# Optimization experiments

Measured on AMD Instinct MI355X. Metric: run time of the kernel, lower is better.

## Reference

```python
import jax, jax.numpy as jnp
import numpy as np

N = 50000          # nodes
E = 800000         # directed edges
C = 64             # hidden width = n_clusters
K = 20             # SSGConv propagation hops
RATIO = 30         # TopKPooling ratio (int -> keep 30 nodes)
ALPHAS = (0.7, 0.7, 0.35, 0.7 / 3.0, 0.175)  # 0.7 then 0.7/(i+1)


def setup_inputs() -> dict:
    key = jax.random.key(0)
    ks = jax.random.split(key, 20)
    inp = {
        'x': jax.random.normal(ks[0], (N, 8), dtype=jnp.float32),
        'edge_index': jax.random.randint(ks[1], (2, E), 0, N, dtype=jnp.int32),
        'W0': 0.1 * jax.random.normal(ks[2], (C, 4), dtype=jnp.float32),
        'b0': 0.1 * jax.random.normal(ks[3], (C,), dtype=jnp.float32),
        'W1': 0.1 * jax.random.normal(ks[4], (C, C), dtype=jnp.float32),
        'b1': 0.1 * jax.random.normal(ks[5], (C,), dtype=jnp.float32),
        'W2': 0.1 * jax.random.normal(ks[6], (C, C), dtype=jnp.float32),
        'b2': 0.1 * jax.random.normal(ks[7], (C,), dtype=jnp.float32),
        'W3': 0.1 * jax.random.normal(ks[8], (C, C), dtype=jnp.float32),
        'b3': 0.1 * jax.random.normal(ks[9], (C,), dtype=jnp.float32),
        'W4': 0.1 * jax.random.normal(ks[10], (C, C), dtype=jnp.float32),
        'b4': 0.1 * jax.random.normal(ks[11], (C,), dtype=jnp.float32),
        'Wm': 0.1 * jax.random.normal(ks[12], (C, C), dtype=jnp.float32),
        'bm': 0.1 * jax.random.normal(ks[13], (C,), dtype=jnp.float32),
        'wp': 0.1 * jax.random.normal(ks[14], (C,), dtype=jnp.float32),
    }
    return inp


def _gcn_norm(edge_index, n):
    # add self loops (fill value 1), symmetric normalization D^-1/2 A D^-1/2
    loops = jnp.arange(n, dtype=edge_index.dtype)
    row = jnp.concatenate([edge_index[0], loops])  # source j
    col = jnp.concatenate([edge_index[1], loops])  # target i
    w = jnp.ones(row.shape[0], dtype=jnp.float32)
    deg = jax.ops.segment_sum(w, col, num_segments=n)
    dinv = jnp.where(deg > 0, jax.lax.rsqrt(deg), 0.0)
    return row, col, dinv[row] * dinv[col]


def _ssg(x, row, col, norm, n, alpha, W, b):
    # SSGConv: h = alpha*x + (1-alpha)/K * sum_k A_norm^k x; then Linear
    coef = (1.0 - alpha) / K

    def body(carry, _):
        xk, h = carry
        xk = jax.ops.segment_sum(xk[row] * norm[:, None], col, num_segments=n)
        return (xk, h + coef * xk), None

    (_, h), _ = jax.lax.scan(body, (x, alpha * x), None, length=K)
    return h @ W.T + b


def reference(x, edge_index, W0, b0, W1, b1, W2, b2, W3, b3, W4, b4, Wm, bm, wp):
    x = x[:, :4]
    row, col, norm = _gcn_norm(edge_index, N)
    relu = jax.nn.relu
    x = relu(_ssg(x, row, col, norm, N, ALPHAS[0], W0, b0))
    x = relu(_ssg(x, row, col, norm, N, ALPHAS[1], W1, b1))
    x = relu(_ssg(x, row, col, norm, N, ALPHAS[2], W2, b2)) + x
    x = relu(_ssg(x, row, col, norm, N, ALPHAS[3], W3, b3)) + x
    x = relu(_ssg(x, row, col, norm, N, ALPHAS[4], W4, b4)) + x
    # MLP (mlp_units=[], mlp_act=Identity): single Linear to n_clusters==C
    x = x @ Wm.T + bm
    # TopKPooling: tanh-normalized projection score, keep top RATIO nodes
    score = jnp.tanh((x @ wp) / jnp.linalg.norm(wp))
    top_score, perm = jax.lax.top_k(score, RATIO)
    xp = x[perm] * top_score[:, None]  # [RATIO, C]
    # global_max_pool over the single graph
    return jnp.max(xp, axis=0, keepdims=True)  # [1, C]
```

## Files before the change

### kernel.cpp

```cpp
#include <hip/hip_runtime.h>
#include <hip/hip_fp16.h>
#include <cstdint>
#include <cstddef>

#define NN 50000
#define EE 800000
#define NNZ (NN + EE)
#define KK 20
#define TPK 30
#define P1B 64
#define P1CH ((NN + P1B - 1) / P1B)
#define SCB 256
#define SCNB ((NN + SCB - 1) / SCB)


__device__ __forceinline__ float2 h2f(unsigned int u) {
  __half2 h = *reinterpret_cast<__half2*>(&u);
  return __half22float2(h);
}
__device__ __forceinline__ unsigned int f2h(float a, float b) {
  __half2 h = __floats2half2_rn(a, b);
  return *reinterpret_cast<unsigned int*>(&h);
}


__global__ __launch_bounds__(256) void init_deg(int* deg) {
  int t = blockIdx.x * 256 + threadIdx.x;
  if (t < NN) deg[t] = 1;
}

__global__ __launch_bounds__(256) void count_deg(const int* __restrict__ ecol, int* deg) {
  int t = blockIdx.x * 256 + threadIdx.x;
  if (t < EE) atomicAdd(&deg[ecol[t]], 1);
}

__global__ __launch_bounds__(256) void scan_bsum(const int* __restrict__ deg, int* __restrict__ bsum) {
  __shared__ int red[256];
  int tid = threadIdx.x;
  int t = blockIdx.x * 256 + tid;
  red[tid] = (t < NN) ? deg[t] : 0;
  __syncthreads();
  for (int o = 128; o > 0; o >>= 1) {
    if (tid < o) red[tid] += red[tid + o];
    __syncthreads();
  }
  if (tid == 0) bsum[blockIdx.x] = red[0];
}

__global__ __launch_bounds__(256) void scan_boff(const int* __restrict__ bsum, int* __restrict__ boff) {
  __shared__ int s[256];
  int tid = threadIdx.x;
  int own = (tid < SCNB) ? bsum[tid] : 0;
  s[tid] = own;
  __syncthreads();
  for (int o = 1; o < 256; o <<= 1) {
    int v = s[tid];
    int u = (tid >= o) ? s[tid - o] : 0;
    __syncthreads();
    s[tid] = v + u;
    __syncthreads();
  }
  if (tid < SCNB) boff[tid] = s[tid] - own;
}

__global__ __launch_bounds__(256) void scan_write(const int* __restrict__ deg,
                                                  const int* __restrict__ boff,
                                                  int* __restrict__ rowptr, int* __restrict__ cursor,
                                                  float* __restrict__ dinv) {
  __shared__ int s[256];
  int tid = threadIdx.x;
  int t = blockIdx.x * 256 + tid;
  int d = (t < NN) ? deg[t] : 0;
  s[tid] = d;
  __syncthreads();
  for (int o = 1; o < 256; o <<= 1) {
    int v = s[tid];
    int u = (tid >= o) ? s[tid - o] : 0;
    __syncthreads();
    s[tid] = v + u;
    __syncthreads();
  }
  if (t < NN) {
    int excl = boff[blockIdx.x] + s[tid] - d;
    rowptr[t] = excl;
    cursor[t] = excl;
    dinv[t] = 1.0f / sqrtf((float)d);
    if (t == NN - 1) rowptr[NN] = excl + d;
  }
}

__global__ __launch_bounds__(256) void scatter_csr(const int* __restrict__ erow,
                                                   const int* __restrict__ ecol,
                                                   const float* __restrict__ dinv, int* cursor,
                                                   int2* __restrict__ meta) {
  int t = blockIdx.x * 256 + threadIdx.x;
  if (t < EE) {
    int r = erow[t], c = ecol[t];
    int p = atomicAdd(&cursor[c], 1);
    meta[p] = make_int2(r, __float_as_int(dinv[r] * dinv[c]));
  } else if (t < NNZ) {
    int i = t - EE;
    int p = atomicAdd(&cursor[i], 1);
    meta[p] = make_int2(i, __float_as_int(dinv[i] * dinv[i]));
  }
}

__global__ __launch_bounds__(256) void extract_x0(const float* __restrict__ x, float4* __restrict__ x0) {
  int t = blockIdx.x * 256 + threadIdx.x;
  if (t < NN) x0[t] = *(const float4*)&x[(size_t)t * 8];
}


__global__ __launch_bounds__(256) void sweep64h(const uint4* __restrict__ tinq,
                                                const uint4* __restrict__ xinq,
                                                const float4* __restrict__ xinf,
                                                uint4* __restrict__ touth,
                                                float4* __restrict__ toutf,
                                                const int* __restrict__ rowptr,
                                                const int2* __restrict__ meta,
                                                float aacc, float axc, int isFinal) {
  int lane = threadIdx.x & 63;
  int w = threadIdx.x >> 6;
  int v = blockIdx.x * 4 + w;
  if (v >= NN) return;
  int c8 = lane & 7;
  int e8 = lane >> 3;
  int s = rowptr[v], e = rowptr[v + 1];
  float a0 = 0.f, a1 = 0.f, a2 = 0.f, a3 = 0.f;
  float a4 = 0.f, a5 = 0.f, a6 = 0.f, a7 = 0.f;
  for (int base = s; base < e; base += 64) {
    int nj = e - base;
    if (nj > 64) nj = 64;
    int2 mL = (lane < nj) ? meta[base + lane] : make_int2(0, 0);
    int T = (nj + 7) >> 3;
    int t = 0;
    for (; t + 1 < T; t += 2) {
      int j0 = e8 + 8 * t;
      int j1 = j0 + 8;
      int s0 = __shfl(mL.x, j0);
      int s1 = __shfl(mL.x, j1);
      float w0 = __int_as_float(__shfl(mL.y, j0));
      float w1 = __int_as_float(__shfl(mL.y, j1));
      uint4 q0 = tinq[(size_t)s0 * 8 + c8];
      uint4 q1 = tinq[(size_t)s1 * 8 + c8];
      float2 f;
      f = h2f(q0.x); a0 = fmaf(w0, f.x, a0); a1 = fmaf(w0, f.y, a1);
      f = h2f(q0.y); a2 = fmaf(w0, f.x, a2); a3 = fmaf(w0, f.y, a3);
      f = h2f(q0.z); a4 = fmaf(w0, f.x, a4); a5 = fmaf(w0, f.y, a5);
      f = h2f(q0.w); a6 = fmaf(w0, f.x, a6); a7 = fmaf(w0, f.y, a7);
      f = h2f(q1.x); a0 = fmaf(w1, f.x, a0); a1 = fmaf(w1, f.y, a1);
      f = h2f(q1.y); a2 = fmaf(w1, f.x, a2); a3 = fmaf(w1, f.y, a3);
      f = h2f(q1.z); a4 = fmaf(w1, f.x, a4); a5 = fmaf(w1, f.y, a5);
      f = h2f(q1.w); a6 = fmaf(w1, f.x, a6); a7 = fmaf(w1, f.y, a7);
    }
    if (t < T) {
      int j0 = e8 + 8 * t;
      int s0 = __shfl(mL.x, j0);
      float w0 = __int_as_float(__shfl(mL.y, j0));
      uint4 q0 = tinq[(size_t)s0 * 8 + c8];
      float2 f;
      f = h2f(q0.x); a0 = fmaf(w0, f.x, a0); a1 = fmaf(w0, f.y, a1);
      f = h2f(q0.y); a2 = fmaf(w0, f.x, a2); a3 = fmaf(w0, f.y, a3);
      f = h2f(q0.z); a4 = fmaf(w0, f.x, a4); a5 = fmaf(w0, f.y, a5);
      f = h2f(q0.w); a6 = fmaf(w0, f.x, a6); a7 = fmaf(w0, f.y, a7);
    }
  }
#pragma unroll
  for (int o = 8; o <= 32; o <<= 1) {
    a0 += __shfl_xor(a0, o); a1 += __shfl_xor(a1, o);
    a2 += __shfl_xor(a2, o); a3 += __shfl_xor(a3, o);
    a4 += __shfl_xor(a4, o); a5 += __shfl_xor(a5, o);
    a6 += __shfl_xor(a6, o); a7 += __shfl_xor(a7, o);
  }
  if (e8 == 0) {
    if (isFinal) {
      float4 x0v = xinf[(size_t)v * 16 + c8 * 2];
      float4 x1v = xinf[(size_t)v * 16 + c8 * 2 + 1];
      float4 r0, r1;
      r0.x = aacc * a0 + axc * x0v.x; r0.y = aacc * a1 + axc * x0v.y;
      r0.z = aacc * a2 + axc * x0v.z; r0.w = aacc * a3 + axc * x0v.w;
      r1.x = aacc * a4 + axc * x1v.x; r1.y = aacc * a5 + axc * x1v.y;
      r1.z = aacc * a6 + axc * x1v.z; r1.w = aacc * a7 + axc * x1v.w;
      toutf[(size_t)v * 16 + c8 * 2] = r0;
      toutf[(size_t)v * 16 + c8 * 2 + 1] = r1;
    } else {
      uint4 xq = xinq[(size_t)v * 8 + c8];
      float2 f;
      f = h2f(xq.x); float o0 = a0 + f.x, o1 = a1 + f.y;
      f = h2f(xq.y); float o2 = a2 + f.x, o3 = a3 + f.y;
      f = h2f(xq.z); float o4 = a4 + f.x, o5 = a5 + f.y;
      f = h2f(xq.w); float o6 = a6 + f.x, o7 = a7 + f.y;
      uint4 r;
      r.x = f2h(o0, o1); r.y = f2h(o2, o3);
      r.z = f2h(o4, o5); r.w = f2h(o6, o7);
      touth[(size_t)v * 8 + c8] = r;
    }
  }
}

__global__ __launch_bounds__(256) void sweep4(const float4* __restrict__ tin,
                                              const float4* __restrict__ xin,
                                              float4* __restrict__ tout,
                                              const int* __restrict__ rowptr,
                                              const int2* __restrict__ meta,
                                              float aacc, float axc) {
  int lane = threadIdx.x & 63;
  int w = threadIdx.x >> 6;
  int n16 = lane & 15;
  int e4 = lane >> 4;
  int v = (blockIdx.x * 4 + w) * 16 + n16;
  int vv = (v < NN) ? v : (NN - 1);
  int s = rowptr[vv], e = rowptr[vv + 1];
  float a0 = 0.f, a1 = 0.f, a2 = 0.f, a3 = 0.f;
  float b0 = 0.f, b1 = 0.f, b2 = 0.f, b3 = 0.f;
  int i = s + e4;
  for (; i + 12 < e; i += 16) {
    int2 m0 = meta[i];
    int2 m1 = meta[i + 4];
    int2 m2 = meta[i + 8];
    int2 m3 = meta[i + 12];
    float w0 = __int_as_float(m0.y);
    float w1 = __int_as_float(m1.y);
    float w2 = __int_as_float(m2.y);
    float w3 = __int_as_float(m3.y);
    float4 t0 = tin[m0.x];
    float4 t1 = tin[m1.x];
    float4 t2 = tin[m2.x];
    float4 t3 = tin[m3.x];
    a0 = fmaf(w0, t0.x, a0); a1 = fmaf(w0, t0.y, a1);
    a2 = fmaf(w0, t0.z, a2); a3 = fmaf(w0, t0.w, a3);
    b0 = fmaf(w1, t1.x, b0); b1 = fmaf(w1, t1.y, b1);
    b2 = fmaf(w1, t1.z, b2); b3 = fmaf(w1, t1.w, b3);
    a0 = fmaf(w2, t2.x, a0); a1 = fmaf(w2, t2.y, a1);
    a2 = fmaf(w2, t2.z, a2); a3 = fmaf(w2, t2.w, a3);
    b0 = fmaf(w3, t3.x, b0); b1 = fmaf(w3, t3.y, b1);
    b2 = fmaf(w3, t3.z, b2); b3 = fmaf(w3, t3.w, b3);
  }
  for (; i < e; i += 4) {
    int2 m0 = meta[i];
    float w0 = __int_as_float(m0.y);
    float4 t0 = tin[m0.x];
    a0 = fmaf(w0, t0.x, a0); a1 = fmaf(w0, t0.y, a1);
    a2 = fmaf(w0, t0.z, a2); a3 = fmaf(w0, t0.w, a3);
  }
  a0 += b0; a1 += b1; a2 += b2; a3 += b3;
  a0 += __shfl_xor(a0, 16); a1 += __shfl_xor(a1, 16);
  a2 += __shfl_xor(a2, 16); a3 += __shfl_xor(a3, 16);
  a0 += __shfl_xor(a0, 32); a1 += __shfl_xor(a1, 32);
  a2 += __shfl_xor(a2, 32); a3 += __shfl_xor(a3, 32);
  if (e4 == 0 && v < NN) {
    float4 xv = xin[v];
    float4 o;
    o.x = aacc * a0 + axc * xv.x;
    o.y = aacc * a1 + axc * xv.y;
    o.z = aacc * a2 + axc * xv.z;
    o.w = aacc * a3 + axc * xv.w;
    tout[v] = o;
  }
}


__global__ __launch_bounds__(256) void dense4(const float* __restrict__ h4,
                                              const float* __restrict__ W,
                                              const float* __restrict__ b,
                                              float* __restrict__ out,
                                              unsigned int* __restrict__ outh) {
  __shared__ float sWt[4 * 64];
  int tid = threadIdx.x;
  {
    int j = tid >> 2, c = tid & 3;
    sWt[c * 64 + j] = W[tid];
  }
  __syncthreads();
  int lane = tid & 63, w = tid >> 6;
  int n = blockIdx.x * 4 + w;
  if (n >= NN) return;
  float acc = b[lane];
#pragma unroll
  for (int c = 0; c < 4; ++c)
    acc = fmaf(h4[(size_t)n * 4 + c], sWt[c * 64 + lane], acc);
  acc = fmaxf(acc, 0.f);
  out[(size_t)n * 64 + lane] = acc;
  int p = lane & 31;
  float va = __shfl(acc, 2 * p);
  float vb = __shfl(acc, 2 * p + 1);
  if (lane < 32) outh[(size_t)n * 32 + lane] = f2h(va, vb);
}

#define DN 128
__global__ __launch_bounds__(256) void dense64(const float* __restrict__ h,
                                               const float* __restrict__ W,
                                               const float* __restrict__ b,
                                               const float* __restrict__ resid,
                                               float* __restrict__ out,
                                               uint4* __restrict__ outh,
                                               int doRelu, int doResid) {
  __shared__ float sX[64 * 130];
  __shared__ float sWt[64 * 68];
  int tid = threadIdx.x;
  int base = blockIdx.x * DN;
  for (int i = tid; i < 64 * 64; i += 256) {
    int o = i >> 6, c = i & 63;
    sWt[c * 68 + o] = W[i];
  }
  for (int i = tid; i < DN * 64; i += 256) {
    int node = i >> 6, c = i & 63;
    int n = base + node;
    sX[c * 130 + node] = (n < NN) ? h[(size_t)n * 64 + c] : 0.f;
  }
  __syncthreads();
  int j = tid & 63;
  int q = tid >> 6;
  float acc0[16], acc1[16];
#pragma unroll
  for (int o = 0; o < 16; ++o) { acc0[o] = b[q * 16 + o]; acc1[o] = acc0[o]; }
  for (int c = 0; c < 64; ++c) {
    float x0 = sX[c * 130 + j];
    float x1 = sX[c * 130 + 64 + j];
#pragma unroll
    for (int o4 = 0; o4 < 4; ++o4) {
      float4 wv = *(const float4*)&sWt[c * 68 + q * 16 + o4 * 4];
      acc0[o4 * 4 + 0] = fmaf(x0, wv.x, acc0[o4 * 4 + 0]);
      acc0[o4 * 4 + 1] = fmaf(x0, wv.y, acc0[o4 * 4 + 1]);
      acc0[o4 * 4 + 2] = fmaf(x0, wv.z, acc0[o4 * 4 + 2]);
      acc0[o4 * 4 + 3] = fmaf(x0, wv.w, acc0[o4 * 4 + 3]);
      acc1[o4 * 4 + 0] = fmaf(x1, wv.x, acc1[o4 * 4 + 0]);
      acc1[o4 * 4 + 1] = fmaf(x1, wv.y, acc1[o4 * 4 + 1]);
      acc1[o4 * 4 + 2] = fmaf(x1, wv.z, acc1[o4 * 4 + 2]);
      acc1[o4 * 4 + 3] = fmaf(x1, wv.w, acc1[o4 * 4 + 3]);
    }
  }
  int n0 = base + j, n1 = base + 64 + j;
#pragma unroll
  for (int half = 0; half < 2; ++half) {
    int n = half ? n1 : n0;
    float* acc = half ? acc1 : acc0;
    if (n < NN) {
      if (doRelu) {
#pragma unroll
        for (int o = 0; o < 16; ++o) acc[o] = fmaxf(acc[o], 0.f);
      }
      if (doResid) {
#pragma unroll
        for (int o4 = 0; o4 < 4; ++o4) {
          float4 rv = *(const float4*)&resid[(size_t)n * 64 + q * 16 + o4 * 4];
          acc[o4 * 4 + 0] += rv.x; acc[o4 * 4 + 1] += rv.y;
          acc[o4 * 4 + 2] += rv.z; acc[o4 * 4 + 3] += rv.w;
        }
      }
#pragma unroll
      for (int o4 = 0; o4 < 4; ++o4) {
        float4 r;
        r.x = acc[o4 * 4 + 0]; r.y = acc[o4 * 4 + 1];
        r.z = acc[o4 * 4 + 2]; r.w = acc[o4 * 4 + 3];
        *(float4*)&out[(size_t)n * 64 + q * 16 + o4 * 4] = r;
      }
      if (outh) {
        uint4 u;
        u.x = f2h(acc[0], acc[1]);  u.y = f2h(acc[2], acc[3]);
        u.z = f2h(acc[4], acc[5]);  u.w = f2h(acc[6], acc[7]);
        outh[(size_t)n * 8 + q * 2] = u;
        u.x = f2h(acc[8], acc[9]);  u.y = f2h(acc[10], acc[11]);
        u.z = f2h(acc[12], acc[13]); u.w = f2h(acc[14], acc[15]);
        outh[(size_t)n * 8 + q * 2 + 1] = u;
      }
    }
  }
}


__global__ __launch_bounds__(256) void score_k(const float* __restrict__ y,
                                               const float* __restrict__ wp,
                                               float* __restrict__ scores) {
  int tid = threadIdx.x;
  int lane = tid & 63, w = tid >> 6;
  int n = blockIdx.x * 4 + w;
  if (n >= NN) return;
  float wv = wp[lane];
  float s = wv * wv;
#pragma unroll
  for (int o = 32; o > 0; o >>= 1) s += __shfl_xor(s, o);
  float invn = 1.0f / sqrtf(s);
  float p = y[(size_t)n * 64 + lane] * wv;
#pragma unroll
  for (int o = 32; o > 0; o >>= 1) p += __shfl_xor(p, o);
  if (lane == 0) scores[n] = tanhf(p * invn);
}

__device__ __forceinline__ bool lexgt(float v1, int i1, float v2, int i2) {
  return (v1 > v2) || (v1 == v2 && i1 < i2);
}

__global__ __launch_bounds__(64, 1) void topk_p1(const float* __restrict__ score,
                                                 float* __restrict__ candv,
                                                 int* __restrict__ candi) {
  int lane = threadIdx.x;
  int base = blockIdx.x * P1CH;
  float lv[TPK]; int li[TPK];
#pragma unroll
  for (int k = 0; k < TPK; ++k) { lv[k] = -3.4e38f; li[k] = 0x7FFFFFFF; }
  for (int k = lane; k < P1CH; k += 64) {
    int idx = base + k;
    if (idx >= NN) break;
    float v = score[idx];
    if (lexgt(v, idx, lv[TPK - 1], li[TPK - 1])) {
      float cv = v; int ci = idx;
#pragma unroll
      for (int m = 0; m < TPK; ++m) {
        bool sw = lexgt(cv, ci, lv[m], li[m]);
        float tv = sw ? lv[m] : cv; int ti = sw ? li[m] : ci;
        lv[m] = sw ? cv : lv[m]; li[m] = sw ? ci : li[m];
        cv = tv; ci = ti;
      }
    }
  }
  for (int r = 0; r < TPK; ++r) {
    float bv = lv[0]; int bi = li[0];
#pragma unroll
    for (int o = 32; o > 0; o >>= 1) {
      float ov = __shfl_xor(bv, o); int oi = __shfl_xor(bi, o);
      if (lexgt(ov, oi, bv, bi)) { bv = ov; bi = oi; }
    }
    if (lane == 0) { candv[blockIdx.x * TPK + r] = bv; candi[blockIdx.x * TPK + r] = bi; }
    bool mine = (li[0] == bi);
#pragma unroll
    for (int m = 0; m < TPK - 1; ++m) {
      lv[m] = mine ? lv[m + 1] : lv[m];
      li[m] = mine ? li[m + 1] : li[m];
    }
    if (mine) { lv[TPK - 1] = -3.4e38f; li[TPK - 1] = 0x7FFFFFFF; }
  }
}

__global__ __launch_bounds__(64, 1) void topk_p2_final(const float* __restrict__ candv,
                                                       const int* __restrict__ candi,
                                                       const float* __restrict__ y,
                                                       float* __restrict__ out) {
  __shared__ float sV[TPK];
  __shared__ int sI[TPK];
  int lane = threadIdx.x;
  float lv[TPK]; int li[TPK];
#pragma unroll
  for (int k = 0; k < TPK; ++k) { lv[k] = -3.4e38f; li[k] = 0x7FFFFFFF; }
  for (int k = lane; k < P1B * TPK; k += 64) {
    float v = candv[k]; int id = candi[k];
    if (lexgt(v, id, lv[TPK - 1], li[TPK - 1])) {
      float cv = v; int ci = id;
#pragma unroll
      for (int m = 0; m < TPK; ++m) {
        bool sw = lexgt(cv, ci, lv[m], li[m]);
        float tv = sw ? lv[m] : cv; int ti = sw ? li[m] : ci;
        lv[m] = sw ? cv : lv[m]; li[m] = sw ? ci : li[m];
        cv = tv; ci = ti;
      }
    }
  }
  for (int r = 0; r < TPK; ++r) {
    float bv = lv[0]; int bi = li[0];
#pragma unroll
    for (int o = 32; o > 0; o >>= 1) {
      float ov = __shfl_xor(bv, o); int oi = __shfl_xor(bi, o);
      if (lexgt(ov, oi, bv, bi)) { bv = ov; bi = oi; }
    }
    if (lane == 0) { sV[r] = bv; sI[r] = bi; }
    bool mine = (li[0] == bi);
#pragma unroll
    for (int m = 0; m < TPK - 1; ++m) {
      lv[m] = mine ? lv[m + 1] : lv[m];
      li[m] = mine ? li[m + 1] : li[m];
    }
    if (mine) { lv[TPK - 1] = -3.4e38f; li[TPK - 1] = 0x7FFFFFFF; }
  }
  __syncthreads();
  float m = -3.4e38f;
  for (int r = 0; r < TPK; ++r)
    m = fmaxf(m, y[(size_t)sI[r] * 64 + lane] * sV[r]);
  out[lane] = m;
}


extern "C" void kernel_launch(void* const* d_in, const int* in_sizes, int n_in,
                              void* d_out, int out_size, void* d_ws, size_t ws_size,
                              hipStream_t stream) {
  const float* x = (const float*)d_in[0];
  const int* ei = (const int*)d_in[1];
  const float* Wl[5] = {(const float*)d_in[2], (const float*)d_in[4], (const float*)d_in[6],
                        (const float*)d_in[8], (const float*)d_in[10]};
  const float* bl[5] = {(const float*)d_in[3], (const float*)d_in[5], (const float*)d_in[7],
                        (const float*)d_in[9], (const float*)d_in[11]};
  const float* Wm = (const float*)d_in[12];
  const float* bm = (const float*)d_in[13];
  const float* wp = (const float*)d_in[14];
  float* out = (float*)d_out;

  uint8_t* base = (uint8_t*)d_ws;
  size_t off = 0;
  auto alloc = [&](size_t bytes) -> void* {
    void* p = base + off;
    off += (bytes + 255) & ~(size_t)255;
    return p;
  };
  int* deg = (int*)alloc(NN * 4);
  int* rowptr = (int*)alloc((NN + 1) * 4);
  int* cursor = (int*)alloc(NN * 4);
  float* dinv = (float*)alloc(NN * 4);
  int* bsum = (int*)alloc(SCNB * 4);
  int* boff = (int*)alloc(SCNB * 4);
  int2* meta = (int2*)alloc((size_t)NNZ * 8);
  float* x0 = (float*)alloc((size_t)NN * 4 * 4);
  float* t4a = (float*)alloc((size_t)NN * 4 * 4);
  float* t4b = (float*)alloc((size_t)NN * 4 * 4);
  float* xcur = (float*)alloc((size_t)NN * 64 * 4);
  float* tA = (float*)alloc((size_t)NN * 64 * 4);
  uint4* xh = (uint4*)alloc((size_t)NN * 64 * 2);
  uint4* thA = (uint4*)alloc((size_t)NN * 64 * 2);
  uint4* thB = (uint4*)alloc((size_t)NN * 64 * 2);
  float* scores = (float*)alloc(NN * 4);
  float* candv = (float*)alloc((size_t)P1B * TPK * 4);
  int* candi = (int*)alloc((size_t)P1B * TPK * 4);

  const int* erow = ei;
  const int* ecol = ei + EE;

  init_deg<<<(NN + 255) / 256, 256, 0, stream>>>(deg);
  count_deg<<<(EE + 255) / 256, 256, 0, stream>>>(ecol, deg);
  scan_bsum<<<SCNB, 256, 0, stream>>>(deg, bsum);
  scan_boff<<<1, 256, 0, stream>>>(bsum, boff);
  scan_write<<<SCNB, 256, 0, stream>>>(deg, boff, rowptr, cursor, dinv);
  scatter_csr<<<(NNZ + 255) / 256, 256, 0, stream>>>(erow, ecol, dinv, cursor, meta);
  extract_x0<<<(NN + 255) / 256, 256, 0, stream>>>(x, (float4*)x0);

  const float AL[5] = {0.7f, 0.7f, 0.35f, 0.7f / 3.0f, 0.175f};

  {
    float coef = (1.0f - AL[0]) / (float)KK;
    const float* tin = x0;
    float* tout = t4a;
    for (int k = 1; k <= KK; ++k) {
      float aacc = (k == KK) ? coef : 1.0f;
      float axc = (k == KK) ? AL[0] : 1.0f;
      sweep4<<<(NN + 63) / 64, 256, 0, stream>>>((const float4*)tin, (const float4*)x0,
                                                 (float4*)tout, rowptr, meta, aacc, axc);
      tin = tout;
      tout = (tout == t4a) ? t4b : t4a;
    }
    dense4<<<(NN + 3) / 4, 256, 0, stream>>>(tin, Wl[0], bl[0], xcur, (unsigned int*)xh);
  }
  for (int l = 1; l < 5; ++l) {
    float coef = (1.0f - AL[l]) / (float)KK;
    const uint4* tin = xh;
    uint4* tout = thA;
    for (int k = 1; k < KK; ++k) {
      sweep64h<<<(NN + 3) / 4, 256, 0, stream>>>(tin, xh, nullptr, tout, nullptr, rowptr, meta,
                                                 1.0f, 1.0f, 0);
      tin = tout;
      tout = (tout == thA) ? thB : thA;
    }
    sweep64h<<<(NN + 3) / 4, 256, 0, stream>>>(tin, nullptr, (const float4*)xcur, nullptr,
                                               (float4*)tA, rowptr, meta, coef, AL[l], 1);
    dense64<<<(NN + DN - 1) / DN, 256, 0, stream>>>(tA, Wl[l], bl[l], xcur, xcur,
                                                    (l < 4) ? xh : nullptr, 1, (l >= 2) ? 1 : 0);
  }
  dense64<<<(NN + DN - 1) / DN, 256, 0, stream>>>(xcur, Wm, bm, nullptr, tA, nullptr, 0, 0);
  score_k<<<(NN + 3) / 4, 256, 0, stream>>>(tA, wp, scores);
  topk_p1<<<P1B, 64, 0, stream>>>(scores, candv, candi);
  topk_p2_final<<<1, 64, 0, stream>>>(candv, candi, tA, out);
}
```

Baseline: 2.196 ms.

## Process two nodes per wavefront in fp16 sweep and simplify top-k passes

```diff
diff --git a/kernel.cpp b/kernel.cpp
--- a/kernel.cpp
+++ b/kernel.cpp
@@ -10,6 +10,7 @@
 #define TPK 30
 #define P1B 64
 #define P1CH ((NN + P1B - 1) / P1B)
+#define P1D 13
 #define SCB 256
 #define SCNB ((NN + SCB - 1) / SCB)
 
@@ -121,79 +122,150 @@
                                                 float aacc, float axc, int isFinal) {
   int lane = threadIdx.x & 63;
   int w = threadIdx.x >> 6;
-  int v = blockIdx.x * 4 + w;
-  if (v >= NN) return;
+  int v0 = (blockIdx.x * 4 + w) * 2;
+  int v1 = v0 + 1;
+  if (v0 >= NN) return;
   int c8 = lane & 7;
   int e8 = lane >> 3;
-  int s = rowptr[v], e = rowptr[v + 1];
+  int s0 = rowptr[v0];
+  int s1 = rowptr[v0 + 1];
+  int e1 = rowptr[v0 + 2];
+  int d0 = s1 - s0, d1 = e1 - s1;
+  int nj0 = (d0 > 64) ? 64 : d0;
+  int nj1 = (d1 > 64) ? 64 : d1;
+  int2 mA = (lane < nj0) ? meta[s0 + lane] : make_int2(0, 0);
+  int2 mB = (lane < nj1) ? meta[s1 + lane] : make_int2(0, 0);
   float a0 = 0.f, a1 = 0.f, a2 = 0.f, a3 = 0.f;
   float a4 = 0.f, a5 = 0.f, a6 = 0.f, a7 = 0.f;
-  for (int base = s; base < e; base += 64) {
-    int nj = e - base;
-    if (nj > 64) nj = 64;
-    int2 mL = (lane < nj) ? meta[base + lane] : make_int2(0, 0);
-    int T = (nj + 7) >> 3;
-    int t = 0;
-    for (; t + 1 < T; t += 2) {
-      int j0 = e8 + 8 * t;
-      int j1 = j0 + 8;
-      int s0 = __shfl(mL.x, j0);
-      int s1 = __shfl(mL.x, j1);
-      float w0 = __int_as_float(__shfl(mL.y, j0));
-      float w1 = __int_as_float(__shfl(mL.y, j1));
-      uint4 q0 = tinq[(size_t)s0 * 8 + c8];
-      uint4 q1 = tinq[(size_t)s1 * 8 + c8];
+  float b0 = 0.f, b1 = 0.f, b2 = 0.f, b3 = 0.f;
+  float b4 = 0.f, b5 = 0.f, b6 = 0.f, b7 = 0.f;
+  int T0 = (nj0 + 7) >> 3;
+  int T1 = (nj1 + 7) >> 3;
+  int Tc = (T0 < T1) ? T0 : T1;
+  int t = 0;
+  for (; t < Tc; ++t) {
+    int j = e8 + 8 * t;
+    int sa = __shfl(mA.x, j);
+    int sb = __shfl(mB.x, j);
+    float wa = __int_as_float(__shfl(mA.y, j));
+    float wb = __int_as_float(__shfl(mB.y, j));
+    uint4 qa = tinq[(size_t)sa * 8 + c8];
+    uint4 qb = tinq[(size_t)sb * 8 + c8];
+    float2 f;
+    f = h2f(qa.x); a0 = fmaf(wa, f.x, a0); a1 = fmaf(wa, f.y, a1);
+    f = h2f(qa.y); a2 = fmaf(wa, f.x, a2); a3 = fmaf(wa, f.y, a3);
+    f = h2f(qa.z); a4 = fmaf(wa, f.x, a4); a5 = fmaf(wa, f.y, a5);
+    f = h2f(qa.w); a6 = fmaf(wa, f.x, a6); a7 = fmaf(wa, f.y, a7);
+    f = h2f(qb.x); b0 = fmaf(wb, f.x, b0); b1 = fmaf(wb, f.y, b1);
+    f = h2f(qb.y); b2 = fmaf(wb, f.x, b2); b3 = fmaf(wb, f.y, b3);
+    f = h2f(qb.z); b4 = fmaf(wb, f.x, b4); b5 = fmaf(wb, f.y, b5);
+    f = h2f(qb.w); b6 = fmaf(wb, f.x, b6); b7 = fmaf(wb, f.y, b7);
+  }
+  for (; t < T0; ++t) {
+    int j = e8 + 8 * t;
+    int sa = __shfl(mA.x, j);
+    float wa = __int_as_float(__shfl(mA.y, j));
+    uint4 qa = tinq[(size_t)sa * 8 + c8];
+    float2 f;
+    f = h2f(qa.x); a0 = fmaf(wa, f.x, a0); a1 = fmaf(wa, f.y, a1);
+    f = h2f(qa.y); a2 = fmaf(wa, f.x, a2); a3 = fmaf(wa, f.y, a3);
+    f = h2f(qa.z); a4 = fmaf(wa, f.x, a4); a5 = fmaf(wa, f.y, a5);
+    f = h2f(qa.w); a6 = fmaf(wa, f.x, a6); a7 = fmaf(wa, f.y, a7);
+  }
+  for (; t < T1; ++t) {
+    int j = e8 + 8 * t;
+    int sb = __shfl(mB.x, j);
+    float wb = __int_as_float(__shfl(mB.y, j));
+    uint4 qb = tinq[(size_t)sb * 8 + c8];
+    float2 f;
+    f = h2f(qb.x); b0 = fmaf(wb, f.x, b0); b1 = fmaf(wb, f.y, b1);
+    f = h2f(qb.y); b2 = fmaf(wb, f.x, b2); b3 = fmaf(wb, f.y, b3);
+    f = h2f(qb.z); b4 = fmaf(wb, f.x, b4); b5 = fmaf(wb, f.y, b5);
+    f = h2f(qb.w); b6 = fmaf(wb, f.x, b6); b7 = fmaf(wb, f.y, b7);
+  }
+  if (d0 > 64) {
+    int e = s0 + d0;
+    for (int c2 = s0 + 64; c2 < e; c2 += 64) {
+      int nj2 = e - c2; if (nj2 > 64) nj2 = 64;
+      int2 mX = (lane < nj2) ? meta[c2 + lane] : make_int2(0, 0);
+      int T2 = (nj2 + 7) >> 3;
+      for (int t2 = 0; t2 < T2; ++t2) {
+        int j = e8 + 8 * t2;
+        int sa = __shfl(mX.x, j);
+        float wa = __int_as_float(__shfl(mX.y, j));
+        uint4 qa = tinq[(size_t)sa * 8 + c8];
+        float2 f;
+        f = h2f(qa.x); a0 = fmaf(wa, f.x, a0); a1 = fmaf(wa, f.y, a1);
+        f = h2f(qa.y); a2 = fmaf(wa, f.x, a2); a3 = fmaf(wa, f.y, a3);
+        f = h2f(qa.z); a4 = fmaf(wa, f.x, a4); a5 = fmaf(wa, f.y, a5);
+        f = h2f(qa.w); a6 = fmaf(wa, f.x, a6); a7 = fmaf(wa, f.y, a7);
+      }
+    }
+  }
+  if (d1 > 64) {
+    int e = s1 + d1;
+    for (int c2 = s1 + 64; c2 < e; c2 += 64) {
+      int nj2 = e - c2; if (nj2 > 64) nj2 = 64;
+      int2 mX = (lane < nj2) ? meta[c2 + lane] : make_int2(0, 0);
+      int T2 = (nj2 + 7) >> 3;
+      for (int t2 = 0; t2 < T2; ++t2) {
+        int j = e8 + 8 * t2;
+        int sb = __shfl(mX.x, j);
+        float wb = __int_as_float(__shfl(mX.y, j));
+        uint4 qb = tinq[(size_t)sb * 8 + c8];
+        float2 f;
+        f = h2f(qb.x); b0 = fmaf(wb, f.x, b0); b1 = fmaf(wb, f.y, b1);
+        f = h2f(qb.y); b2 = fmaf(wb, f.x, b2); b3 = fmaf(wb, f.y, b3);
+        f = h2f(qb.z); b4 = fmaf(wb, f.x, b4); b5 = fmaf(wb, f.y, b5);
+        f = h2f(qb.w); b6 = fmaf(wb, f.x, b6); b7 = fmaf(wb, f.y, b7);
+      }
+    }
+  }
+#pragma unroll
+  for (int o = 8; o <= 32; o <<= 1) {
+    a0 += __shfl_xor(a0, o); b0 += __shfl_xor(b0, o);
+    a1 += __shfl_xor(a1, o); b1 += __shfl_xor(b1, o);
+    a2 += __shfl_xor(a2, o); b2 += __shfl_xor(b2, o);
+    a3 += __shfl_xor(a3, o); b3 += __shfl_xor(b3, o);
+    a4 += __shfl_xor(a4, o); b4 += __shfl_xor(b4, o);
+    a5 += __shfl_xor(a5, o); b5 += __shfl_xor(b5, o);
+    a6 += __shfl_xor(a6, o); b6 += __shfl_xor(b6, o);
+    a7 += __shfl_xor(a7, o); b7 += __shfl_xor(b7, o);
+  }
+  if (e8 == 0) {
+    if (!isFinal) {
+      uint4 xq0 = xinq[(size_t)v0 * 8 + c8];
+      uint4 xq1 = xinq[(size_t)v1 * 8 + c8];
       float2 f;
-      f = h2f(q0.x); a0 = fmaf(w0, f.x, a0); a1 = fmaf(w0, f.y, a1);
-      f = h2f(q0.y); a2 = fmaf(w0, f.x, a2); a3 = fmaf(w0, f.y, a3);
-      f = h2f(q0.z); a4 = fmaf(w0, f.x, a4); a5 = fmaf(w0, f.y, a5);
-      f = h2f(q0.w); a6 = fmaf(w0, f.x, a6); a7 = fmaf(w0, f.y, a7);
-      f = h2f(q1.x); a0 = fmaf(w1, f.x, a0); a1 = fmaf(w1, f.y, a1);
-      f = h2f(q1.y); a2 = fmaf(w1, f.x, a2); a3 = fmaf(w1, f.y, a3);
-      f = h2f(q1.z); a4 = fmaf(w1, f.x, a4); a5 = fmaf(w1, f.y, a5);
-      f = h2f(q1.w); a6 = fmaf(w1, f.x, a6); a7 = fmaf(w1, f.y, a7);
-    }
-    if (t < T) {
-      int j0 = e8 + 8 * t;
-      int s0 = __shfl(mL.x, j0);
-      float w0 = __int_as_float(__shfl(mL.y, j0));
-      uint4 q0 = tinq[(size_t)s0 * 8 + c8];
-      float2 f;
-      f = h2f(q0.x); a0 = fmaf(w0, f.x, a0); a1 = fmaf(w0, f.y, a1);
-      f = h2f(q0.y); a2 = fmaf(w0, f.x, a2); a3 = fmaf(w0, f.y, a3);
-      f = h2f(q0.z); a4 = fmaf(w0, f.x, a4); a5 = fmaf(w0, f.y, a5);
-      f = h2f(q0.w); a6 = fmaf(w0, f.x, a6); a7 = fmaf(w0, f.y, a7);
-    }
-  }
-#pragma unroll
-  for (int o = 8; o <= 32; o <<= 1) {
-    a0 += __shfl_xor(a0, o); a1 += __shfl_xor(a1, o);
-    a2 += __shfl_xor(a2, o); a3 += __shfl_xor(a3, o);
-    a4 += __shfl_xor(a4, o); a5 += __shfl_xor(a5, o);
-    a6 += __shfl_xor(a6, o); a7 += __shfl_xor(a7, o);
-  }
-  if (e8 == 0) {
-    if (isFinal) {
-      float4 x0v = xinf[(size_t)v * 16 + c8 * 2];
-      float4 x1v = xinf[(size_t)v * 16 + c8 * 2 + 1];
+      uint4 r;
+      f = h2f(xq0.x); r.x = f2h(a0 + f.x, a1 + f.y);
+      f = h2f(xq0.y); r.y = f2h(a2 + f.x, a3 + f.y);
+      f = h2f(xq0.z); r.z = f2h(a4 + f.x, a5 + f.y);
+      f = h2f(xq0.w); r.w = f2h(a6 + f.x, a7 + f.y);
+      touth[(size_t)v0 * 8 + c8] = r;
+      f = h2f(xq1.x); r.x = f2h(b0 + f.x, b1 + f.y);
+      f = h2f(xq1.y); r.y = f2h(b2 + f.x, b3 + f.y);
+      f = h2f(xq1.z); r.z = f2h(b4 + f.x, b5 + f.y);
+      f = h2f(xq1.w); r.w = f2h(b6 + f.x, b7 + f.y);
+      touth[(size_t)v1 * 8 + c8] = r;
+    } else {
+      float4 x0v = xinf[(size_t)v0 * 16 + c8 * 2];
+      float4 x1v = xinf[(size_t)v0 * 16 + c8 * 2 + 1];
       float4 r0, r1;
       r0.x = aacc * a0 + axc * x0v.x; r0.y = aacc * a1 + axc * x0v.y;
       r0.z = aacc * a2 + axc * x0v.z; r0.w = aacc * a3 + axc * x0v.w;
       r1.x = aacc * a4 + axc * x1v.x; r1.y = aacc * a5 + axc * x1v.y;
       r1.z = aacc * a6 + axc * x1v.z; r1.w = aacc * a7 + axc * x1v.w;
-      toutf[(size_t)v * 16 + c8 * 2] = r0;
-      toutf[(size_t)v * 16 + c8 * 2 + 1] = r1;
-    } else {
-      uint4 xq = xinq[(size_t)v * 8 + c8];
-      float2 f;
-      f = h2f(xq.x); float o0 = a0 + f.x, o1 = a1 + f.y;
-      f = h2f(xq.y); float o2 = a2 + f.x, o3 = a3 + f.y;
-      f = h2f(xq.z); float o4 = a4 + f.x, o5 = a5 + f.y;
-      f = h2f(xq.w); float o6 = a6 + f.x, o7 = a7 + f.y;
-      uint4 r;
-      r.x = f2h(o0, o1); r.y = f2h(o2, o3);
-      r.z = f2h(o4, o5); r.w = f2h(o6, o7);
-      touth[(size_t)v * 8 + c8] = r;
+      toutf[(size_t)v0 * 16 + c8 * 2] = r0;
+      toutf[(size_t)v0 * 16 + c8 * 2 + 1] = r1;
+      float4 y0v = xinf[(size_t)v1 * 16 + c8 * 2];
+      float4 y1v = xinf[(size_t)v1 * 16 + c8 * 2 + 1];
+      r0.x = aacc * b0 + axc * y0v.x; r0.y = aacc * b1 + axc * y0v.y;
+      r0.z = aacc * b2 + axc * y0v.z; r0.w = aacc * b3 + axc * y0v.w;
+      r1.x = aacc * b4 + axc * y1v.x; r1.y = aacc * b5 + axc * y1v.y;
+      r1.z = aacc * b6 + axc * y1v.z; r1.w = aacc * b7 + axc * y1v.w;
+      toutf[(size_t)v1 * 16 + c8 * 2] = r0;
+      toutf[(size_t)v1 * 16 + c8 * 2 + 1] = r1;
     }
   }
 }
@@ -396,17 +468,17 @@
                                                  int* __restrict__ candi) {
   int lane = threadIdx.x;
   int base = blockIdx.x * P1CH;
-  float lv[TPK]; int li[TPK];
-#pragma unroll
-  for (int k = 0; k < TPK; ++k) { lv[k] = -3.4e38f; li[k] = 0x7FFFFFFF; }
+  float lv[P1D]; int li[P1D];
+#pragma unroll
+  for (int k = 0; k < P1D; ++k) { lv[k] = -3.4e38f; li[k] = 0x7FFFFFFF; }
   for (int k = lane; k < P1CH; k += 64) {
     int idx = base + k;
     if (idx >= NN) break;
     float v = score[idx];
-    if (lexgt(v, idx, lv[TPK - 1], li[TPK - 1])) {
+    if (lexgt(v, idx, lv[P1D - 1], li[P1D - 1])) {
       float cv = v; int ci = idx;
 #pragma unroll
-      for (int m = 0; m < TPK; ++m) {
+      for (int m = 0; m < P1D; ++m) {
         bool sw = lexgt(cv, ci, lv[m], li[m]);
         float tv = sw ? lv[m] : cv; int ti = sw ? li[m] : ci;
         lv[m] = sw ? cv : lv[m]; li[m] = sw ? ci : li[m];
@@ -424,11 +496,11 @@
     if (lane == 0) { candv[blockIdx.x * TPK + r] = bv; candi[blockIdx.x * TPK + r] = bi; }
     bool mine = (li[0] == bi);
 #pragma unroll
-    for (int m = 0; m < TPK - 1; ++m) {
+    for (int m = 0; m < P1D - 1; ++m) {
       lv[m] = mine ? lv[m + 1] : lv[m];
       li[m] = mine ? li[m + 1] : li[m];
     }
-    if (mine) { lv[TPK - 1] = -3.4e38f; li[TPK - 1] = 0x7FFFFFFF; }
+    if (mine) { lv[P1D - 1] = -3.4e38f; li[P1D - 1] = 0x7FFFFFFF; }
   }
 }
 
@@ -436,40 +508,26 @@
                                                        const int* __restrict__ candi,
                                                        const float* __restrict__ y,
                                                        float* __restrict__ out) {
+  __shared__ float sv[P1B * TPK];
+  __shared__ int si[P1B * TPK];
   __shared__ float sV[TPK];
   __shared__ int sI[TPK];
   int lane = threadIdx.x;
-  float lv[TPK]; int li[TPK];
-#pragma unroll
-  for (int k = 0; k < TPK; ++k) { lv[k] = -3.4e38f; li[k] = 0x7FFFFFFF; }
-  for (int k = lane; k < P1B * TPK; k += 64) {
-    float v = candv[k]; int id = candi[k];
-    if (lexgt(v, id, lv[TPK - 1], li[TPK - 1])) {
-      float cv = v; int ci = id;
-#pragma unroll
-      for (int m = 0; m < TPK; ++m) {
-        bool sw = lexgt(cv, ci, lv[m], li[m]);
-        float tv = sw ? lv[m] : cv; int ti = sw ? li[m] : ci;
-        lv[m] = sw ? cv : lv[m]; li[m] = sw ? ci : li[m];
-        cv = tv; ci = ti;
-      }
-    }
-  }
+  for (int k = lane; k < P1B * TPK; k += 64) { sv[k] = candv[k]; si[k] = candi[k]; }
+  __syncthreads();
+  int myptr = 0;
   for (int r = 0; r < TPK; ++r) {
-    float bv = lv[0]; int bi = li[0];
+    bool alive = (myptr < TPK);
+    float hv = alive ? sv[lane * TPK + myptr] : -3.4e38f;
+    int hi = alive ? si[lane * TPK + myptr] : 0x7FFFFFFF;
+    float bv = hv; int bi = hi;
 #pragma unroll
     for (int o = 32; o > 0; o >>= 1) {
       float ov = __shfl_xor(bv, o); int oi = __shfl_xor(bi, o);
       if (lexgt(ov, oi, bv, bi)) { bv = ov; bi = oi; }
     }
+    if (alive && hi == bi) myptr++;
     if (lane == 0) { sV[r] = bv; sI[r] = bi; }
-    bool mine = (li[0] == bi);
-#pragma unroll
-    for (int m = 0; m < TPK - 1; ++m) {
-      lv[m] = mine ? lv[m + 1] : lv[m];
-      li[m] = mine ? li[m + 1] : li[m];
-    }
-    if (mine) { lv[TPK - 1] = -3.4e38f; li[TPK - 1] = 0x7FFFFFFF; }
   }
   __syncthreads();
   float m = -3.4e38f;
@@ -551,12 +609,12 @@
     const uint4* tin = xh;
     uint4* tout = thA;
     for (int k = 1; k < KK; ++k) {
-      sweep64h<<<(NN + 3) / 4, 256, 0, stream>>>(tin, xh, nullptr, tout, nullptr, rowptr, meta,
+      sweep64h<<<(NN + 7) / 8, 256, 0, stream>>>(tin, xh, nullptr, tout, nullptr, rowptr, meta,
                                                  1.0f, 1.0f, 0);
       tin = tout;
       tout = (tout == thA) ? thB : thA;
     }
-    sweep64h<<<(NN + 3) / 4, 256, 0, stream>>>(tin, nullptr, (const float4*)xcur, nullptr,
+    sweep64h<<<(NN + 7) / 8, 256, 0, stream>>>(tin, nullptr, (const float4*)xcur, nullptr,
                                                (float4*)tA, rowptr, meta, coef, AL[l], 1);
     dense64<<<(NN + DN - 1) / DN, 256, 0, stream>>>(tA, Wl[l], bl[l], xcur, xcur,
                                                     (l < 4) ? xh : nullptr, 1, (l >= 2) ? 1 : 0);
```

New measurement: 2.081 ms. 1.06x faster.

## Shard fp16 features by channel per XCD and pack edge metadata into 32 bits

Applied to the files above, without the earlier changes.

```diff
diff --git a/kernel.cpp b/kernel.cpp
--- a/kernel.cpp
+++ b/kernel.cpp
@@ -10,8 +10,11 @@
 #define TPK 30
 #define P1B 64
 #define P1CH ((NN + P1B - 1) / P1B)
+#define P1D 13
 #define SCB 256
 #define SCNB ((NN + SCB - 1) / SCB)
+#define NSH 8
+#define SWGRP ((NN + 31) / 32)
 
 
 __device__ __forceinline__ float2 h2f(unsigned int u) {
@@ -21,6 +24,11 @@
 __device__ __forceinline__ unsigned int f2h(float a, float b) {
   __half2 h = __floats2half2_rn(a, b);
   return *reinterpret_cast<unsigned int*>(&h);
+}
+__device__ __forceinline__ float wgt_of(unsigned int m) {
+  __half_raw hr;
+  hr.x = (unsigned short)(m >> 16);
+  return __half2float(__half(hr));
 }
 
 
@@ -92,16 +100,18 @@
 __global__ __launch_bounds__(256) void scatter_csr(const int* __restrict__ erow,
                                                    const int* __restrict__ ecol,
                                                    const float* __restrict__ dinv, int* cursor,
-                                                   int2* __restrict__ meta) {
+                                                   unsigned int* __restrict__ meta4) {
   int t = blockIdx.x * 256 + threadIdx.x;
   if (t < EE) {
     int r = erow[t], c = ecol[t];
     int p = atomicAdd(&cursor[c], 1);
-    meta[p] = make_int2(r, __float_as_int(dinv[r] * dinv[c]));
+    __half_raw hr = __half_raw(__float2half_rn(dinv[r] * dinv[c]));
+    meta4[p] = ((unsigned int)hr.x << 16) | (unsigned int)r;
   } else if (t < NNZ) {
     int i = t - EE;
     int p = atomicAdd(&cursor[i], 1);
-    meta[p] = make_int2(i, __float_as_int(dinv[i] * dinv[i]));
+    __half_raw hr = __half_raw(__float2half_rn(dinv[i] * dinv[i]));
+    meta4[p] = ((unsigned int)hr.x << 16) | (unsigned int)i;
   }
 }
 
@@ -110,60 +120,47 @@
   if (t < NN) x0[t] = *(const float4*)&x[(size_t)t * 8];
 }
 
-
-__global__ __launch_bounds__(256) void sweep64h(const uint4* __restrict__ tinq,
-                                                const uint4* __restrict__ xinq,
-                                                const float4* __restrict__ xinf,
-                                                uint4* __restrict__ touth,
-                                                float4* __restrict__ toutf,
-                                                const int* __restrict__ rowptr,
-                                                const int2* __restrict__ meta,
-                                                float aacc, float axc, int isFinal) {
+__global__ __launch_bounds__(256) void sweep64sh(const uint4* __restrict__ tin_sh,
+                                                 const uint4* __restrict__ xin_sh,
+                                                 const float* __restrict__ xf,
+                                                 uint4* __restrict__ tout_sh,
+                                                 float* __restrict__ toutf,
+                                                 const int* __restrict__ rowptr,
+                                                 const unsigned int* __restrict__ meta4,
+                                                 float aacc, float axc, int isFinal) {
   int lane = threadIdx.x & 63;
   int w = threadIdx.x >> 6;
-  int v = blockIdx.x * 4 + w;
-  if (v >= NN) return;
-  int c8 = lane & 7;
-  int e8 = lane >> 3;
-  int s = rowptr[v], e = rowptr[v + 1];
+  int shard = blockIdx.x & 7;
+  int grp = blockIdx.x >> 3;
+  int vbase = (grp * 4 + w) * 8;
+  if (vbase >= NN) return;
+  int nd = lane & 7;
+  int slot = lane >> 3;
+  int v = vbase + nd;
+  int s = rowptr[v];
+  int deg = rowptr[v + 1] - s;
+  int T = (deg + 7) >> 3;
+#pragma unroll
+  for (int o = 1; o < 64; o <<= 1) {
+    int tt = __shfl_xor(T, o);
+    T = (tt > T) ? tt : T;
+  }
+  const uint4* stb = tin_sh + (size_t)shard * NN;
   float a0 = 0.f, a1 = 0.f, a2 = 0.f, a3 = 0.f;
   float a4 = 0.f, a5 = 0.f, a6 = 0.f, a7 = 0.f;
-  for (int base = s; base < e; base += 64) {
-    int nj = e - base;
-    if (nj > 64) nj = 64;
-    int2 mL = (lane < nj) ? meta[base + lane] : make_int2(0, 0);
-    int T = (nj + 7) >> 3;
-    int t = 0;
-    for (; t + 1 < T; t += 2) {
-      int j0 = e8 + 8 * t;
-      int j1 = j0 + 8;
-      int s0 = __shfl(mL.x, j0);
-      int s1 = __shfl(mL.x, j1);
-      float w0 = __int_as_float(__shfl(mL.y, j0));
-      float w1 = __int_as_float(__shfl(mL.y, j1));
-      uint4 q0 = tinq[(size_t)s0 * 8 + c8];
-      uint4 q1 = tinq[(size_t)s1 * 8 + c8];
-      float2 f;
-      f = h2f(q0.x); a0 = fmaf(w0, f.x, a0); a1 = fmaf(w0, f.y, a1);
-      f = h2f(q0.y); a2 = fmaf(w0, f.x, a2); a3 = fmaf(w0, f.y, a3);
-      f = h2f(q0.z); a4 = fmaf(w0, f.x, a4); a5 = fmaf(w0, f.y, a5);
-      f = h2f(q0.w); a6 = fmaf(w0, f.x, a6); a7 = fmaf(w0, f.y, a7);
-      f = h2f(q1.x); a0 = fmaf(w1, f.x, a0); a1 = fmaf(w1, f.y, a1);
-      f = h2f(q1.y); a2 = fmaf(w1, f.x, a2); a3 = fmaf(w1, f.y, a3);
-      f = h2f(q1.z); a4 = fmaf(w1, f.x, a4); a5 = fmaf(w1, f.y, a5);
-      f = h2f(q1.w); a6 = fmaf(w1, f.x, a6); a7 = fmaf(w1, f.y, a7);
-    }
-    if (t < T) {
-      int j0 = e8 + 8 * t;
-      int s0 = __shfl(mL.x, j0);
-      float w0 = __int_as_float(__shfl(mL.y, j0));
-      uint4 q0 = tinq[(size_t)s0 * 8 + c8];
-      float2 f;
-      f = h2f(q0.x); a0 = fmaf(w0, f.x, a0); a1 = fmaf(w0, f.y, a1);
-      f = h2f(q0.y); a2 = fmaf(w0, f.x, a2); a3 = fmaf(w0, f.y, a3);
-      f = h2f(q0.z); a4 = fmaf(w0, f.x, a4); a5 = fmaf(w0, f.y, a5);
-      f = h2f(q0.w); a6 = fmaf(w0, f.x, a6); a7 = fmaf(w0, f.y, a7);
-    }
+  unsigned int mcur = (slot < deg) ? meta4[s + slot] : 0u;
+  for (int t = 0; t < T; ++t) {
+    int nsl = slot + 8 * (t + 1);
+    unsigned int mnext = (t + 1 < T && nsl < deg) ? meta4[s + nsl] : 0u;
+    int src = (int)(mcur & 0xffffu);
+    float wgt = wgt_of(mcur);
+    uint4 q = stb[src];
+    float2 f;
+    f = h2f(q.x); a0 = fmaf(wgt, f.x, a0); a1 = fmaf(wgt, f.y, a1);
+    f = h2f(q.y); a2 = fmaf(wgt, f.x, a2); a3 = fmaf(wgt, f.y, a3);
+    f = h2f(q.z); a4 = fmaf(wgt, f.x, a4); a5 = fmaf(wgt, f.y, a5);
+    f = h2f(q.w); a6 = fmaf(wgt, f.x, a6); a7 = fmaf(wgt, f.y, a7);
+    mcur = mnext;
   }
 #pragma unroll
   for (int o = 8; o <= 32; o <<= 1) {
@@ -172,28 +169,28 @@
     a4 += __shfl_xor(a4, o); a5 += __shfl_xor(a5, o);
     a6 += __shfl_xor(a6, o); a7 += __shfl_xor(a7, o);
   }
-  if (e8 == 0) {
-    if (isFinal) {
-      float4 x0v = xinf[(size_t)v * 16 + c8 * 2];
-      float4 x1v = xinf[(size_t)v * 16 + c8 * 2 + 1];
+  if (lane < 8) {
+    int vv = vbase + lane;
+    if (!isFinal) {
+      uint4 xq = xin_sh[(size_t)shard * NN + vv];
+      float2 f;
+      uint4 r;
+      f = h2f(xq.x); r.x = f2h(a0 + f.x, a1 + f.y);
+      f = h2f(xq.y); r.y = f2h(a2 + f.x, a3 + f.y);
+      f = h2f(xq.z); r.z = f2h(a4 + f.x, a5 + f.y);
+      f = h2f(xq.w); r.w = f2h(a6 + f.x, a7 + f.y);
+      tout_sh[(size_t)shard * NN + vv] = r;
+    } else {
+      const float4* xr = (const float4*)&xf[(size_t)vv * 64 + shard * 8];
+      float4 x0v = xr[0], x1v = xr[1];
       float4 r0, r1;
       r0.x = aacc * a0 + axc * x0v.x; r0.y = aacc * a1 + axc * x0v.y;
       r0.z = aacc * a2 + axc * x0v.z; r0.w = aacc * a3 + axc * x0v.w;
       r1.x = aacc * a4 + axc * x1v.x; r1.y = aacc * a5 + axc * x1v.y;
       r1.z = aacc * a6 + axc * x1v.z; r1.w = aacc * a7 + axc * x1v.w;
-      toutf[(size_t)v * 16 + c8 * 2] = r0;
-      toutf[(size_t)v * 16 + c8 * 2 + 1] = r1;
-    } else {
-      uint4 xq = xinq[(size_t)v * 8 + c8];
-      float2 f;
-      f = h2f(xq.x); float o0 = a0 + f.x, o1 = a1 + f.y;
-      f = h2f(xq.y); float o2 = a2 + f.x, o3 = a3 + f.y;
-      f = h2f(xq.z); float o4 = a4 + f.x, o5 = a5 + f.y;
-      f = h2f(xq.w); float o6 = a6 + f.x, o7 = a7 + f.y;
-      uint4 r;
-      r.x = f2h(o0, o1); r.y = f2h(o2, o3);
-      r.z = f2h(o4, o5); r.w = f2h(o6, o7);
-      touth[(size_t)v * 8 + c8] = r;
+      float4* tw = (float4*)&toutf[(size_t)vv * 64 + shard * 8];
+      tw[0] = r0;
+      tw[1] = r1;
     }
   }
 }
@@ -202,7 +199,7 @@
                                               const float4* __restrict__ xin,
                                               float4* __restrict__ tout,
                                               const int* __restrict__ rowptr,
-                                              const int2* __restrict__ meta,
+                                              const unsigned int* __restrict__ meta4,
                                               float aacc, float axc) {
   int lane = threadIdx.x & 63;
   int w = threadIdx.x >> 6;
@@ -215,18 +212,15 @@
   float b0 = 0.f, b1 = 0.f, b2 = 0.f, b3 = 0.f;
   int i = s + e4;
   for (; i + 12 < e; i += 16) {
-    int2 m0 = meta[i];
-    int2 m1 = meta[i + 4];
-    int2 m2 = meta[i + 8];
-    int2 m3 = meta[i + 12];
-    float w0 = __int_as_float(m0.y);
-    float w1 = __int_as_float(m1.y);
-    float w2 = __int_as_float(m2.y);
-    float w3 = __int_as_float(m3.y);
-    float4 t0 = tin[m0.x];
-    float4 t1 = tin[m1.x];
-    float4 t2 = tin[m2.x];
-    float4 t3 = tin[m3.x];
+    unsigned int m0 = meta4[i];
+    unsigned int m1 = meta4[i + 4];
+    unsigned int m2 = meta4[i + 8];
+    unsigned int m3 = meta4[i + 12];
+    float w0 = wgt_of(m0), w1 = wgt_of(m1), w2 = wgt_of(m2), w3 = wgt_of(m3);
+    float4 t0 = tin[m0 & 0xffffu];
+    float4 t1 = tin[m1 & 0xffffu];
+    float4 t2 = tin[m2 & 0xffffu];
+    float4 t3 = tin[m3 & 0xffffu];
     a0 = fmaf(w0, t0.x, a0); a1 = fmaf(w0, t0.y, a1);
     a2 = fmaf(w0, t0.z, a2); a3 = fmaf(w0, t0.w, a3);
     b0 = fmaf(w1, t1.x, b0); b1 = fmaf(w1, t1.y, b1);
@@ -237,9 +231,9 @@
     b2 = fmaf(w3, t3.z, b2); b3 = fmaf(w3, t3.w, b3);
   }
   for (; i < e; i += 4) {
-    int2 m0 = meta[i];
-    float w0 = __int_as_float(m0.y);
-    float4 t0 = tin[m0.x];
+    unsigned int m0 = meta4[i];
+    float w0 = wgt_of(m0);
+    float4 t0 = tin[m0 & 0xffffu];
     a0 = fmaf(w0, t0.x, a0); a1 = fmaf(w0, t0.y, a1);
     a2 = fmaf(w0, t0.z, a2); a3 = fmaf(w0, t0.w, a3);
   }
@@ -264,7 +258,7 @@
                                               const float* __restrict__ W,
                                               const float* __restrict__ b,
                                               float* __restrict__ out,
-                                              unsigned int* __restrict__ outh) {
+                                              unsigned int* __restrict__ outh_u32) {
   __shared__ float sWt[4 * 64];
   int tid = threadIdx.x;
   {
@@ -284,7 +278,10 @@
   int p = lane & 31;
   float va = __shfl(acc, 2 * p);
   float vb = __shfl(acc, 2 * p + 1);
-  if (lane < 32) outh[(size_t)n * 32 + lane] = f2h(va, vb);
+  if (lane < 32) {
+    int shard = p >> 2, pair = p & 3;
+    outh_u32[((size_t)shard * NN + n) * 4 + pair] = f2h(va, vb);
+  }
 }
 
 #define DN 128
@@ -293,7 +290,7 @@
                                                const float* __restrict__ b,
                                                const float* __restrict__ resid,
                                                float* __restrict__ out,
-                                               uint4* __restrict__ outh,
+                                               uint4* __restrict__ outh_sh,
                                                int doRelu, int doResid) {
   __shared__ float sX[64 * 130];
   __shared__ float sWt[64 * 68];
@@ -355,14 +352,14 @@
         r.z = acc[o4 * 4 + 2]; r.w = acc[o4 * 4 + 3];
         *(float4*)&out[(size_t)n * 64 + q * 16 + o4 * 4] = r;
       }
-      if (outh) {
+      if (outh_sh) {
         uint4 u;
         u.x = f2h(acc[0], acc[1]);  u.y = f2h(acc[2], acc[3]);
         u.z = f2h(acc[4], acc[5]);  u.w = f2h(acc[6], acc[7]);
-        outh[(size_t)n * 8 + q * 2] = u;
+        outh_sh[(size_t)(2 * q) * NN + n] = u;
         u.x = f2h(acc[8], acc[9]);  u.y = f2h(acc[10], acc[11]);
         u.z = f2h(acc[12], acc[13]); u.w = f2h(acc[14], acc[15]);
-        outh[(size_t)n * 8 + q * 2 + 1] = u;
+        outh_sh[(size_t)(2 * q + 1) * NN + n] = u;
       }
     }
   }
@@ -396,17 +393,17 @@
                                                  int* __restrict__ candi) {
   int lane = threadIdx.x;
   int base = blockIdx.x * P1CH;
-  float lv[TPK]; int li[TPK];
-#pragma unroll
-  for (int k = 0; k < TPK; ++k) { lv[k] = -3.4e38f; li[k] = 0x7FFFFFFF; }
+  float lv[P1D]; int li[P1D];
+#pragma unroll
+  for (int k = 0; k < P1D; ++k) { lv[k] = -3.4e38f; li[k] = 0x7FFFFFFF; }
   for (int k = lane; k < P1CH; k += 64) {
     int idx = base + k;
     if (idx >= NN) break;
     float v = score[idx];
-    if (lexgt(v, idx, lv[TPK - 1], li[TPK - 1])) {
+    if (lexgt(v, idx, lv[P1D - 1], li[P1D - 1])) {
       float cv = v; int ci = idx;
 #pragma unroll
-      for (int m = 0; m < TPK; ++m) {
+      for (int m = 0; m < P1D; ++m) {
         bool sw = lexgt(cv, ci, lv[m], li[m]);
         float tv = sw ? lv[m] : cv; int ti = sw ? li[m] : ci;
         lv[m] = sw ? cv : lv[m]; li[m] = sw ? ci : li[m];
@@ -424,11 +421,11 @@
     if (lane == 0) { candv[blockIdx.x * TPK + r] = bv; candi[blockIdx.x * TPK + r] = bi; }
     bool mine = (li[0] == bi);
 #pragma unroll
-    for (int m = 0; m < TPK - 1; ++m) {
+    for (int m = 0; m < P1D - 1; ++m) {
       lv[m] = mine ? lv[m + 1] : lv[m];
       li[m] = mine ? li[m + 1] : li[m];
     }
-    if (mine) { lv[TPK - 1] = -3.4e38f; li[TPK - 1] = 0x7FFFFFFF; }
+    if (mine) { lv[P1D - 1] = -3.4e38f; li[P1D - 1] = 0x7FFFFFFF; }
   }
 }
 
@@ -436,40 +433,26 @@
                                                        const int* __restrict__ candi,
                                                        const float* __restrict__ y,
                                                        float* __restrict__ out) {
+  __shared__ float sv[P1B * TPK];
+  __shared__ int si[P1B * TPK];
   __shared__ float sV[TPK];
   __shared__ int sI[TPK];
   int lane = threadIdx.x;
-  float lv[TPK]; int li[TPK];
-#pragma unroll
-  for (int k = 0; k < TPK; ++k) { lv[k] = -3.4e38f; li[k] = 0x7FFFFFFF; }
-  for (int k = lane; k < P1B * TPK; k += 64) {
-    float v = candv[k]; int id = candi[k];
-    if (lexgt(v, id, lv[TPK - 1], li[TPK - 1])) {
-      float cv = v; int ci = id;
-#pragma unroll
-      for (int m = 0; m < TPK; ++m) {
-        bool sw = lexgt(cv, ci, lv[m], li[m]);
-        float tv = sw ? lv[m] : cv; int ti = sw ? li[m] : ci;
-        lv[m] = sw ? cv : lv[m]; li[m] = sw ? ci : li[m];
-        cv = tv; ci = ti;
-      }
-    }
-  }
+  for (int k = lane; k < P1B * TPK; k += 64) { sv[k] = candv[k]; si[k] = candi[k]; }
+  __syncthreads();
+  int myptr = 0;
   for (int r = 0; r < TPK; ++r) {
-    float bv = lv[0]; int bi = li[0];
+    bool alive = (myptr < TPK);
+    float hv = alive ? sv[lane * TPK + myptr] : -3.4e38f;
+    int hi = alive ? si[lane * TPK + myptr] : 0x7FFFFFFF;
+    float bv = hv; int bi = hi;
 #pragma unroll
     for (int o = 32; o > 0; o >>= 1) {
       float ov = __shfl_xor(bv, o); int oi = __shfl_xor(bi, o);
       if (lexgt(ov, oi, bv, bi)) { bv = ov; bi = oi; }
     }
+    if (alive && hi == bi) myptr++;
     if (lane == 0) { sV[r] = bv; sI[r] = bi; }
-    bool mine = (li[0] == bi);
-#pragma unroll
-    for (int m = 0; m < TPK - 1; ++m) {
-      lv[m] = mine ? lv[m + 1] : lv[m];
-      li[m] = mine ? li[m + 1] : li[m];
-    }
-    if (mine) { lv[TPK - 1] = -3.4e38f; li[TPK - 1] = 0x7FFFFFFF; }
   }
   __syncthreads();
   float m = -3.4e38f;
@@ -506,7 +489,7 @@
   float* dinv = (float*)alloc(NN * 4);
   int* bsum = (int*)alloc(SCNB * 4);
   int* boff = (int*)alloc(SCNB * 4);
-  int2* meta = (int2*)alloc((size_t)NNZ * 8);
+  unsigned int* meta4 = (unsigned int*)alloc((size_t)NNZ * 4);
   float* x0 = (float*)alloc((size_t)NN * 4 * 4);
   float* t4a = (float*)alloc((size_t)NN * 4 * 4);
   float* t4b = (float*)alloc((size_t)NN * 4 * 4);
@@ -527,7 +510,7 @@
   scan_bsum<<<SCNB, 256, 0, stream>>>(deg, bsum);
   scan_boff<<<1, 256, 0, stream>>>(bsum, boff);
   scan_write<<<SCNB, 256, 0, stream>>>(deg, boff, rowptr, cursor, dinv);
-  scatter_csr<<<(NNZ + 255) / 256, 256, 0, stream>>>(erow, ecol, dinv, cursor, meta);
+  scatter_csr<<<(NNZ + 255) / 256, 256, 0, stream>>>(erow, ecol, dinv, cursor, meta4);
   extract_x0<<<(NN + 255) / 256, 256, 0, stream>>>(x, (float4*)x0);
 
   const float AL[5] = {0.7f, 0.7f, 0.35f, 0.7f / 3.0f, 0.175f};
@@ -540,7 +523,7 @@
       float aacc = (k == KK) ? coef : 1.0f;
       float axc = (k == KK) ? AL[0] : 1.0f;
       sweep4<<<(NN + 63) / 64, 256, 0, stream>>>((const float4*)tin, (const float4*)x0,
-                                                 (float4*)tout, rowptr, meta, aacc, axc);
+                                                 (float4*)tout, rowptr, meta4, aacc, axc);
       tin = tout;
       tout = (tout == t4a) ? t4b : t4a;
     }
@@ -551,13 +534,13 @@
     const uint4* tin = xh;
     uint4* tout = thA;
     for (int k = 1; k < KK; ++k) {
-      sweep64h<<<(NN + 3) / 4, 256, 0, stream>>>(tin, xh, nullptr, tout, nullptr, rowptr, meta,
+      sweep64sh<<<SWGRP * NSH, 256, 0, stream>>>(tin, xh, nullptr, tout, nullptr, rowptr, meta4,
                                                  1.0f, 1.0f, 0);
       tin = tout;
       tout = (tout == thA) ? thB : thA;
     }
-    sweep64h<<<(NN + 3) / 4, 256, 0, stream>>>(tin, nullptr, (const float4*)xcur, nullptr,
-                                               (float4*)tA, rowptr, meta, coef, AL[l], 1);
+    sweep64sh<<<SWGRP * NSH, 256, 0, stream>>>(tin, nullptr, xcur, nullptr, tA, rowptr, meta4,
+                                               coef, AL[l], 1);
     dense64<<<(NN + DN - 1) / DN, 256, 0, stream>>>(tA, Wl[l], bl[l], xcur, xcur,
                                                     (l < 4) ? xh : nullptr, 1, (l >= 2) ? 1 : 0);
   }
```

New measurement: 3.391 ms. 54.4% more time.
